# Kernel tuning notes

Hardware: AMD Instinct MI355X
Metric: run time of the kernel (lower is better)

The kernel has to match this reference:

```python
import jax, jax.numpy as jnp
import numpy as np

NUM_HEADS = 16
THETA = 10000.0


def _rope(x, cos, sin):
    # x: [B, H, S, d_k]; cos/sin: [S, d_k//2]
    x_even = x[..., 0::2]
    x_odd = x[..., 1::2]
    out_even = x_even * cos - x_odd * sin
    out_odd = x_odd * cos + x_even * sin
    # interleave back to original even/odd layout
    return jnp.stack([out_even, out_odd], axis=-1).reshape(x.shape)


def setup_inputs() -> dict:
    key = jax.random.key(0)
    ks = jax.random.split(key, 5)
    B, S, D = 2, 2048, 1024
    std = 2.0 / (D + D)
    return {
        "x": jax.random.normal(ks[0], (B, S, D), dtype=jnp.float32),
        "w_q": jax.random.normal(ks[1], (D, D), dtype=jnp.float32) * std,
        "w_k": jax.random.normal(ks[2], (D, D), dtype=jnp.float32) * std,
        "w_v": jax.random.normal(ks[3], (D, D), dtype=jnp.float32) * std,
        "w_o": jax.random.normal(ks[4], (D, D), dtype=jnp.float32) * std,
    }


def reference(x, w_q, w_k, w_v, w_o):
    B, S, D = x.shape
    H = NUM_HEADS
    d_k = D // H

    # QKV projections: x @ W.T
    q = jnp.einsum('bsd,ed->bse', x, w_q).reshape(B, S, H, d_k).transpose(0, 2, 1, 3)
    k = jnp.einsum('bsd,ed->bse', x, w_k).reshape(B, S, H, d_k).transpose(0, 2, 1, 3)
    v = jnp.einsum('bsd,ed->bse', x, w_v).reshape(B, S, H, d_k).transpose(0, 2, 1, 3)

    # RoPE (token_positions = arange(S))
    pos = jnp.arange(S, dtype=jnp.float32)
    inv_freq = 1.0 / (THETA ** (2.0 * jnp.arange(d_k // 2, dtype=jnp.float32) / d_k))
    angles = pos[:, None] * inv_freq[None, :]  # [S, d_k//2]
    cos, sin = jnp.cos(angles), jnp.sin(angles)
    q = _rope(q, cos, sin)
    k = _rope(k, cos, sin)

    # causal attention
    scores = jnp.einsum('bhqd,bhkd->bhqk', q, k) / jnp.sqrt(jnp.float32(d_k))
    causal = jnp.tril(jnp.ones((S, S), dtype=bool))
    scores = jnp.where(causal[None, None], scores, -jnp.inf)
    attn = jax.nn.softmax(scores, axis=-1)
    out = jnp.einsum('bhqk,bhkd->bhqd', attn, v)  # [B, H, S, d_k]

    out = out.transpose(0, 2, 1, 3).reshape(B, S, D)
    return jnp.einsum('bsd,ed->bse', out, w_o)
```

## Files before the change

### kernel.cpp

```cpp
#include <hip/hip_runtime.h>

typedef unsigned short u16;
typedef unsigned int u32;
typedef short bf16x8 __attribute__((ext_vector_type(8)));
typedef float f32x4 __attribute__((ext_vector_type(4)));

#define CSC 0.18033688011112042f

__device__ __forceinline__ u16 f2bf(float f) {
    union { float f; unsigned u; } x; x.f = f;
    unsigned r = x.u + 0x7fffu + ((x.u >> 16) & 1u);
    return (u16)(r >> 16);
}
__device__ __forceinline__ float bf2f(u16 v) {
    union { unsigned u; float f; } x; x.u = ((unsigned)v) << 16;
    return x.f;
}
__device__ __forceinline__ u32 cvt_pk_bf16(float lo, float hi) {
    u32 r;
    asm("v_cvt_pk_bf16_f32 %0, %1, %2" : "=v"(r) : "v"(lo), "v"(hi));
    return r;
}
__device__ __forceinline__ float exp2_fast(float x) {
#if __has_builtin(__builtin_amdgcn_exp2f)
    return __builtin_amdgcn_exp2f(x);
#else
    return exp2f(x);
#endif
}
__device__ __forceinline__ void gl_lds16(const u16* g, u16* l) {
#if __has_builtin(__builtin_amdgcn_global_load_lds)
    __builtin_amdgcn_global_load_lds(
        (const __attribute__((address_space(1))) unsigned int*)g,
        (__attribute__((address_space(3))) unsigned int*)l, 16, 0, 0);
#else
    *(bf16x8*)l = *(const bf16x8*)g;
#endif
}
__device__ __forceinline__ int ileave(int x) {
    return (x < 16) ? (x << 1) : (((x - 16) << 1) | 1);
}

__global__ void cvt_all_kernel(const float* __restrict__ x, const float* __restrict__ wq,
                               const float* __restrict__ wk, const float* __restrict__ wv,
                               const float* __restrict__ wo,
                               u16* __restrict__ xb, u16* __restrict__ qkvw,
                               u16* __restrict__ ow) {
    int i = blockIdx.x * 256 + threadIdx.x;
    const float4* src;
    ushort4* dst;
    if (i < 1048576) {
        src = (const float4*)x + i;
        dst = (ushort4*)xb + i;
    } else {
        int r = i - 1048576;
        int m = r >> 18;
        int off = r & 262143;
        const float* s4 = (m == 0) ? wq : (m == 1) ? wk : (m == 2) ? wv : wo;
        u16* d = (m < 3) ? (qkvw + (size_t)m * 1048576) : ow;
        src = (const float4*)s4 + off;
        dst = (ushort4*)d + off;
    }
    float4 v = *src;
    ushort4 o;
    o.x = f2bf(v.x); o.y = f2bf(v.y); o.z = f2bf(v.z); o.w = f2bf(v.w);
    *dst = o;
}

__global__ void rope_kernel(u16* __restrict__ qb, u16* __restrict__ kb) {
    int idx = blockIdx.x * 256 + threadIdx.x;
    u16* buf;
    float scale;
    if (blockIdx.y == 0) { buf = qb; scale = CSC; } else { buf = kb; scale = 1.0f; }
    int g   = idx & 7;
    int row = idx >> 3;
    int s   = row & 2047;
    u16* p = buf + (size_t)row * 64 + g * 8;
    bf16x8 v = *(bf16x8*)p;
    bf16x8 o;
    #pragma unroll
    for (int q = 0; q < 4; ++q) {
        int i = g * 4 + q;
        float inv = exp2_fast((float)i * -0.4152410118609203f);
        float ang = (float)s * inv;
        float sn, cs;
        sincosf(ang, &sn, &cs);
        float e  = bf2f(((u16*)&v)[2 * q]);
        float od = bf2f(((u16*)&v)[2 * q + 1]);
        ((u16*)&o)[2 * q]     = f2bf((e * cs - od * sn) * scale);
        ((u16*)&o)[2 * q + 1] = f2bf((od * cs + e * sn) * scale);
    }
    *(bf16x8*)p = o;
}

__global__ __launch_bounds__(256) void gemm_qkv(const u16* __restrict__ A,
                                                const u16* __restrict__ Bw,
                                                u16* __restrict__ C, int K) {
    __shared__ __align__(16) u16 SB[16384];
    u16* SH = SB;
    const int tid  = threadIdx.x;
    const int bm   = blockIdx.x * 128;
    const int bn   = blockIdx.y * 128;
    const int wave = tid >> 6, lane = tid & 63;
    const int wm   = (wave >> 1) * 64, wn = (wave & 1) * 64;
    const int l16  = lane & 15, quad = lane >> 4;
    const int mat  = bn >> 10;

    f32x4 acc[4][4];
    #pragma unroll
    for (int i = 0; i < 4; i++)
        #pragma unroll
        for (int j = 0; j < 4; j++)
            #pragma unroll
            for (int e = 0; e < 4; e++) acc[i][j][e] = 0.0f;

    const int srow = tid >> 2;
    const int scol = (((tid & 3) ^ ((tid >> 3) & 3))) * 8;
    const u16* gA0 = A  + (size_t)(bm + srow) * K + scol;
    const u16* gA1 = A  + (size_t)(bm + 64 + srow) * K + scol;
    const u16* gB0 = Bw + (size_t)(bn + srow) * K + scol;
    const u16* gB1 = Bw + (size_t)(bn + 64 + srow) * K + scol;
    const int csw = (quad ^ ((l16 >> 1) & 3)) * 8;

    auto stage = [&](int k0, int buf) {
        u16* As = SB + buf * 8192;
        u16* Bs = As + 4096;
        gl_lds16(gA0 + k0, As + (size_t)tid * 8);
        gl_lds16(gA1 + k0, As + (size_t)(tid + 256) * 8);
        gl_lds16(gB0 + k0, Bs + (size_t)tid * 8);
        gl_lds16(gB1 + k0, Bs + (size_t)(tid + 256) * 8);
    };

    stage(0, 0);
    int cur = 0;
    for (int k0 = 0; k0 < K; k0 += 32) {
        __syncthreads();
        if (k0 + 32 < K) stage(k0 + 32, cur ^ 1);
        const u16* As = SB + cur * 8192;
        const u16* Bs = As + 4096;
        bf16x8 af[4], bfr[4];
        #pragma unroll
        for (int i = 0; i < 4; i++) af[i]  = *(const bf16x8*)&As[(wm + i * 16 + l16) * 32 + csw];
        #pragma unroll
        for (int j = 0; j < 4; j++) bfr[j] = *(const bf16x8*)&Bs[(wn + j * 16 + l16) * 32 + csw];
        #pragma unroll
        for (int i = 0; i < 4; i++)
            #pragma unroll
            for (int j = 0; j < 4; j++)
                acc[i][j] = __builtin_amdgcn_mfma_f32_16x16x32_bf16(af[i], bfr[j], acc[i][j], 0, 0, 0);
        cur ^= 1;
    }

    const int b  = bm >> 11, sb = bm & 2047;
    if (mat < 2) {
        #pragma unroll
        for (int pass = 0; pass < 2; ++pass) {
            __syncthreads();
            if ((wn >> 6) == pass) {
                #pragma unroll
                for (int i = 0; i < 4; i++)
                    #pragma unroll
                    for (int j = 0; j < 4; j++)
                        #pragma unroll
                        for (int r = 0; r < 4; r++) {
                            int rl = wm + i * 16 + quad * 4 + r;
                            int cl = j * 16 + l16;
                            SH[rl * 66 + cl] = f2bf(acc[i][j][r]);
                        }
            }
            __syncthreads();
            int rl   = tid >> 1;
            int half = (tid & 1) * 32;
            int c    = (bn + pass * 64) & 1023;
            int h    = c >> 6;
            int s    = sb + rl;
            u16* dst = C + (size_t)mat * 4194304 +
                       (((size_t)(b * 16 + h) * 2048 + s) * 64) + half;
            const u16* srcp = &SH[rl * 66 + half];
            #pragma unroll
            for (int kk = 0; kk < 4; ++kk)
                *(bf16x8*)(dst + kk * 8) = *(const bf16x8*)(srcp + kk * 8);
        }
    } else {
        #pragma unroll
        for (int pass = 0; pass < 2; ++pass) {
            __syncthreads();
            if ((wn >> 6) == pass) {
                #pragma unroll
                for (int i = 0; i < 4; i++)
                    #pragma unroll
                    for (int j = 0; j < 4; j++)
                        #pragma unroll
                        for (int r = 0; r < 4; r++) {
                            int row = j * 16 + l16;
                            int ml  = wm + i * 16 + quad * 4 + r;
                            int sp  = (ml & ~31) | ileave(ml & 31);
                            SH[row * 130 + sp] = f2bf(acc[i][j][r]);
                        }
            }
            __syncthreads();
            int row = tid >> 2, seg = tid & 3;
            int cc  = (bn + pass * 64 + row) & 1023;
            int h = cc >> 6, dv = cc & 63;
            u16* dst = C + (size_t)8388608 +
                       (((size_t)(b * 16 + h) * 64 + dv) * 2048) + sb + seg * 32;
            const u16* srcp = &SH[row * 130 + seg * 32];
            #pragma unroll
            for (int kk = 0; kk < 4; ++kk)
                *(bf16x8*)(dst + kk * 8) = *(const bf16x8*)(srcp + kk * 8);
        }
    }
}

__global__ __launch_bounds__(256, 2) void gemm_out(const u16* __restrict__ A,
                                                   const u16* __restrict__ Bw,
                                                   float* __restrict__ C, int K) {
    __shared__ __align__(16) u16 SB[12288];
    const int tid  = threadIdx.x;
    const int bm   = blockIdx.x * 128;
    const int bn   = blockIdx.y * 64;
    const int wave = tid >> 6, lane = tid & 63;
    const int wm   = wave * 32;
    const int l16  = lane & 15, quad = lane >> 4;

    f32x4 acc[2][4];
    #pragma unroll
    for (int i = 0; i < 2; i++)
        #pragma unroll
        for (int j = 0; j < 4; j++)
            #pragma unroll
            for (int e = 0; e < 4; e++) acc[i][j][e] = 0.0f;

    const int srow = tid >> 2;
    const int scol = (((tid & 3) ^ ((tid >> 3) & 3))) * 8;
    const u16* gA0 = A  + (size_t)(bm + srow) * K + scol;
    const u16* gA1 = A  + (size_t)(bm + 64 + srow) * K + scol;
    const u16* gB0 = Bw + (size_t)(bn + srow) * K + scol;
    const int csw = (quad ^ ((l16 >> 1) & 3)) * 8;

    auto stage = [&](int k0, int buf) {
        u16* base = SB + buf * 6144;
        gl_lds16(gA0 + k0, base + (size_t)tid * 8);
        gl_lds16(gA1 + k0, base + (size_t)(tid + 256) * 8);
        gl_lds16(gB0 + k0, base + 4096 + (size_t)tid * 8);
    };

    stage(0, 0);
    int cur = 0;
    for (int k0 = 0; k0 < K; k0 += 32) {
        __syncthreads();
        if (k0 + 32 < K) stage(k0 + 32, cur ^ 1);
        const u16* As = SB + cur * 6144;
        const u16* Bs = As + 4096;
        bf16x8 af[2], bfr[4];
        #pragma unroll
        for (int i = 0; i < 2; i++) af[i]  = *(const bf16x8*)&As[(wm + i * 16 + l16) * 32 + csw];
        #pragma unroll
        for (int j = 0; j < 4; j++) bfr[j] = *(const bf16x8*)&Bs[(j * 16 + l16) * 32 + csw];
        #pragma unroll
        for (int i = 0; i < 2; i++)
            #pragma unroll
            for (int j = 0; j < 4; j++)
                acc[i][j] = __builtin_amdgcn_mfma_f32_16x16x32_bf16(af[i], bfr[j], acc[i][j], 0, 0, 0);
        cur ^= 1;
    }

    #pragma unroll
    for (int i = 0; i < 2; i++)
        #pragma unroll
        for (int j = 0; j < 4; j++)
            #pragma unroll
            for (int r = 0; r < 4; r++) {
                int mr = bm + wm + i * 16 + quad * 4 + r;
                int nc = bn + j * 16 + l16;
                C[(size_t)mr * 1024 + nc] = acc[i][j][r];
            }
}

__global__ __launch_bounds__(256, 2) void attn_kernel(const u16* __restrict__ Q,
                                                      const u16* __restrict__ Kb,
                                                      const u16* __restrict__ Vt,
                                                      u16* __restrict__ Oout) {
    __shared__ __align__(16) u16 KV[2][8192];
    __shared__ __align__(16) u16 PW[8 * 1024];
    const int tid  = threadIdx.x;
    const int wave = tid >> 6, lane = tid & 63;
    const int l16  = lane & 15, quad = lane >> 4;
    const int bid  = blockIdx.x;
    const int j    = (bid >> 3) & 15;
    const int bh   = (bid & 7) * 4 + (bid >> 7);
    const int T    = 32 - j;
    const int qA0  = j * 64 + wave * 16;
    const int qB0  = (31 - j) * 64 + wave * 16;

    const u16* Qh = Q  + (size_t)bh * 2048 * 64;
    const u16* Kh = Kb + (size_t)bh * 2048 * 64;
    const u16* Vh = Vt + (size_t)bh * 64 * 2048;

    bf16x8 qAf0 = *(const bf16x8*)&Qh[(size_t)(qA0 + l16) * 64 + quad * 8];
    bf16x8 qAf1 = *(const bf16x8*)&Qh[(size_t)(qA0 + l16) * 64 + 32 + quad * 8];
    bf16x8 qBf0 = *(const bf16x8*)&Qh[(size_t)(qB0 + l16) * 64 + quad * 8];
    bf16x8 qBf1 = *(const bf16x8*)&Qh[(size_t)(qB0 + l16) * 64 + 32 + quad * 8];

    f32x4 oA[4], oB[4];
    float lsA[4], lsB[4];
    #pragma unroll
    for (int t = 0; t < 4; t++)
        #pragma unroll
        for (int e = 0; e < 4; e++) { oA[t][e] = 0.0f; oB[t][e] = 0.0f; }
    #pragma unroll
    for (int r = 0; r < 4; r++) { lsA[r] = 0.0f; lsB[r] = 0.0f; }

    const int srow = tid >> 2;
    const int scs  = (((tid & 3) ^ ((tid >> 3) & 3))) * 8;
    const u16* gK = Kh + (size_t)srow * 64 + scs;
    const u16* gV = Vh + (size_t)srow * 2048 + scs;

    const int cswz = (quad ^ ((l16 >> 1) & 3)) * 8;
    const int psw0 = ((quad ^ (l16 & 7)) << 3);
    const int psw1 = (((quad ^ (l16 & 7)) ^ 4) << 3);

    u16* pw16B = PW + wave * 2048;
    u16* pw16A = pw16B + 1024;
    u32* pw32B = (u32*)pw16B;
    u32* pw32A = (u32*)pw16A;

    auto stage = [&](int t, int buf) {
        u16* base = KV[buf];
        gl_lds16(gK + (size_t)t * 4096,      base + (size_t)tid * 8);
        gl_lds16(gK + (size_t)t * 4096 + 32, base + 2048 + (size_t)tid * 8);
        gl_lds16(gV + (size_t)t * 64,        base + 4096 + (size_t)tid * 8);
        gl_lds16(gV + (size_t)t * 64 + 32,   base + 6144 + (size_t)tid * 8);
    };

    auto qk_pack = [&](const bf16x8& q0f, const bf16x8& q1f, bf16x8* kf0, bf16x8* kf1,
                       float* ls, u32* pw32, int q0, int kbase, bool diag) {
        f32x4 s[4];
        #pragma unroll
        for (int n = 0; n < 4; n++) {
            #pragma unroll
            for (int e = 0; e < 4; e++) s[n][e] = 0.0f;
            s[n] = __builtin_amdgcn_mfma_f32_16x16x32_bf16(q0f, kf0[n], s[n], 0, 0, 0);
            s[n] = __builtin_amdgcn_mfma_f32_16x16x32_bf16(q1f, kf1[n], s[n], 0, 0, 0);
        }
        float p[4][4];
        #pragma unroll
        for (int n = 0; n < 4; n++)
            #pragma unroll
            for (int r = 0; r < 4; r++) {
                float v = exp2_fast(s[n][r]);
                if (diag) {
                    int row = q0 + quad * 4 + r;
                    v = (kbase + n * 16 + l16 > row) ? 0.0f : v;
                }
                p[n][r] = v;
                ls[r] += v;
            }
        #pragma unroll
        for (int c = 0; c < 2; c++)
            #pragma unroll
            for (int r = 0; r < 4; r++) {
                int prow = quad * 4 + r;
                int pj   = (((c * 4 + (l16 >> 2)) ^ (prow & 7)) << 2) | (l16 & 3);
                pw32[prow * 32 + pj] = cvt_pk_bf16(p[2 * c][r], p[2 * c + 1][r]);
            }
    };

    auto pv = [&](u16* pw16, bf16x8* vf0, bf16x8* vf1, f32x4* o) {
        bf16x8 pf0 = *(const bf16x8*)&pw16[l16 * 64 + psw0];
        bf16x8 pf1 = *(const bf16x8*)&pw16[l16 * 64 + psw1];
        #pragma unroll
        for (int dn = 0; dn < 4; dn++) {
            o[dn] = __builtin_amdgcn_mfma_f32_16x16x32_bf16(pf0, vf0[dn], o[dn], 0, 0, 0);
            o[dn] = __builtin_amdgcn_mfma_f32_16x16x32_bf16(pf1, vf1[dn], o[dn], 0, 0, 0);
        }
    };

    stage(0, 0);
    for (int t = 0; t < T; ++t) {
        __syncthreads();
        if (t + 1 < T) stage(t + 1, (t + 1) & 1);
        const u16* B = KV[t & 1];
        bf16x8 kf0[4], kf1[4], vf0[4], vf1[4];
        #pragma unroll
        for (int n = 0; n < 4; n++) {
            int ri = (n * 16 + l16) * 32 + cswz;
            kf0[n] = *(const bf16x8*)&B[ri];
            kf1[n] = *(const bf16x8*)&B[2048 + ri];
            vf0[n] = *(const bf16x8*)&B[4096 + ri];
            vf1[n] = *(const bf16x8*)&B[6144 + ri];
        }
        const int kbase = t * 64;
        const bool hasA = (t <= j);

        qk_pack(qBf0, qBf1, kf0, kf1, lsB, pw32B, qB0, kbase, t == T - 1);
        if (hasA)
            qk_pack(qAf0, qAf1, kf0, kf1, lsA, pw32A, qA0, kbase, t == j);

        asm volatile("s_waitcnt lgkmcnt(0)" ::: "memory");

        pv(pw16B, vf0, vf1, oB);
        if (hasA)
            pv(pw16A, vf0, vf1, oA);
    }

    #pragma unroll
    for (int off = 1; off < 16; off <<= 1)
        #pragma unroll
        for (int r = 0; r < 4; r++) {
            lsA[r] += __shfl_xor(lsA[r], off);
            lsB[r] += __shfl_xor(lsB[r], off);
        }

    const int b = bh >> 4, h = bh & 15;
    #pragma unroll
    for (int r = 0; r < 4; r++) {
        float iA = 1.0f / lsA[r];
        float iB = 1.0f / lsB[r];
        int sA = qA0 + quad * 4 + r;
        int sB = qB0 + quad * 4 + r;
        #pragma unroll
        for (int dn = 0; dn < 4; dn++) {
            int d = h * 64 + dn * 16 + l16;
            Oout[((size_t)b * 2048 + sA) * 1024 + d] = f2bf(oA[dn][r] * iA);
            Oout[((size_t)b * 2048 + sB) * 1024 + d] = f2bf(oB[dn][r] * iB);
        }
    }
}

extern "C" void kernel_launch(void* const* d_in, const int* in_sizes, int n_in,
                              void* d_out, int out_size, void* d_ws, size_t ws_size,
                              hipStream_t stream) {
    const float* x  = (const float*)d_in[0];
    const float* wq = (const float*)d_in[1];
    const float* wk = (const float*)d_in[2];
    const float* wv = (const float*)d_in[3];
    const float* wo = (const float*)d_in[4];
    float* out = (float*)d_out;

    const int M = 4096, D = 1024;
    u16* xb    = (u16*)d_ws;
    u16* qkvw  = xb   + (size_t)M * D;
    u16* ow    = qkvw + (size_t)3 * D * D;
    u16* qkv   = ow   + (size_t)D * D;
    u16* qb    = qkv;
    u16* kb    = qkv + (size_t)M * D;
    u16* vtb   = qkv + (size_t)2 * M * D;
    u16* aob   = qkv + (size_t)3 * M * D;

    cvt_all_kernel<<<8192, 256, 0, stream>>>(x, wq, wk, wv, wo, xb, qkvw, ow);

    dim3 gq(32, 24);
    gemm_qkv<<<gq, 256, 0, stream>>>(xb, qkvw, qkv, D);

    dim3 gr(2048, 2);
    rope_kernel<<<gr, 256, 0, stream>>>(qb, kb);

    attn_kernel<<<512, 256, 0, stream>>>(qb, kb, vtb, aob);

    dim3 go(32, 16);
    gemm_out<<<go, 256, 0, stream>>>(aob, ow, out, D);
}
```

Before: 183.6 us.

## Software-pipeline PV of previous tile with QK of current tile

Double-buffers the per-wave P scratch in shared memory and defers each tile's P·V MFMAs to the next iteration, so they run alongside the current tile's QK and exp work. This removes the explicit lgkmcnt wait between writing P and reading it back. In exchange, V fragments for the previous tile are carried in extra registers and the P scratch doubles in size, which may raise register pressure and hurt occupancy at launch bounds of 2.

```diff
diff --git a/kernel.cpp b/kernel.cpp
--- a/kernel.cpp
+++ b/kernel.cpp
@@ -282,7 +282,7 @@
                                                       const u16* __restrict__ Vt,
                                                       u16* __restrict__ Oout) {
     __shared__ __align__(16) u16 KV[2][8192];
-    __shared__ __align__(16) u16 PW[8 * 1024];
+    __shared__ __align__(16) u16 PW[4 * 4096];
     const int tid  = threadIdx.x;
     const int wave = tid >> 6, lane = tid & 63;
     const int l16  = lane & 15, quad = lane >> 4;
@@ -320,10 +320,7 @@
     const int psw0 = ((quad ^ (l16 & 7)) << 3);
     const int psw1 = (((quad ^ (l16 & 7)) ^ 4) << 3);
 
-    u16* pw16B = PW + wave * 2048;
-    u16* pw16A = pw16B + 1024;
-    u32* pw32B = (u32*)pw16B;
-    u32* pw32A = (u32*)pw16A;
+    u16* pwBase = PW + wave * 4096;
 
     auto stage = [&](int t, int buf) {
         u16* base = KV[buf];
@@ -366,7 +363,7 @@
             }
     };
 
-    auto pv = [&](u16* pw16, bf16x8* vf0, bf16x8* vf1, f32x4* o) {
+    auto pv = [&](const u16* pw16, bf16x8* vf0, bf16x8* vf1, f32x4* o) {
         bf16x8 pf0 = *(const bf16x8*)&pw16[l16 * 64 + psw0];
         bf16x8 pf1 = *(const bf16x8*)&pw16[l16 * 64 + psw1];
         #pragma unroll
@@ -375,6 +372,9 @@
             o[dn] = __builtin_amdgcn_mfma_f32_16x16x32_bf16(pf1, vf1[dn], o[dn], 0, 0, 0);
         }
     };
+
+    bf16x8 vfp0[4], vfp1[4];
+    bool prevA = false;
 
     stage(0, 0);
     for (int t = 0; t < T; ++t) {
@@ -390,18 +390,30 @@
             vf0[n] = *(const bf16x8*)&B[4096 + ri];
             vf1[n] = *(const bf16x8*)&B[6144 + ri];
         }
+
+        if (t > 0) {
+            const u16* pp = pwBase + ((t - 1) & 1) * 2048;
+            pv(pp, vfp0, vfp1, oB);
+            if (prevA) pv(pp + 1024, vfp0, vfp1, oA);
+        }
+
         const int kbase = t * 64;
         const bool hasA = (t <= j);
-
-        qk_pack(qBf0, qBf1, kf0, kf1, lsB, pw32B, qB0, kbase, t == T - 1);
+        u32* pwc = (u32*)(pwBase + (t & 1) * 2048);
+
+        qk_pack(qBf0, qBf1, kf0, kf1, lsB, pwc, qB0, kbase, t == T - 1);
         if (hasA)
-            qk_pack(qAf0, qAf1, kf0, kf1, lsA, pw32A, qA0, kbase, t == j);
-
-        asm volatile("s_waitcnt lgkmcnt(0)" ::: "memory");
-
-        pv(pw16B, vf0, vf1, oB);
-        if (hasA)
-            pv(pw16A, vf0, vf1, oA);
+            qk_pack(qAf0, qAf1, kf0, kf1, lsA, pwc + 512, qA0, kbase, t == j);
+
+        #pragma unroll
+        for (int n = 0; n < 4; n++) { vfp0[n] = vf0[n]; vfp1[n] = vf1[n]; }
+        prevA = hasA;
+    }
+
+    {
+        const u16* pp = pwBase + ((T - 1) & 1) * 2048;
+        pv(pp, vfp0, vfp1, oB);
+        if (prevA) pv(pp + 1024, vfp0, vfp1, oA);
     }
 
     #pragma unroll
```

After: 186.8 us. About the same (+1.7%).

## Split attention query tiles across two wave groups in 512-thread blocks

Applied to the files above, without the earlier changes.

The attention kernel now launches 512 threads per block. Waves 0-3 handle the late query tile and waves 4-7 handle the early one, where previously each wave processed both tiles serially. K staging is done by the first 256 threads and V staging by the rest, and each wave keeps only one set of accumulators. This raises parallelism and cuts per-wave register pressure. The cost is that the early-tile waves sit idle after their causal range ends while still joining every barrier, and the larger blocks may reduce how many blocks fit per CU.

```diff
diff --git a/kernel.cpp b/kernel.cpp
--- a/kernel.cpp
+++ b/kernel.cpp
@@ -277,7 +277,7 @@
             }
 }
 
-__global__ __launch_bounds__(256, 2) void attn_kernel(const u16* __restrict__ Q,
+__global__ __launch_bounds__(512, 2) void attn_kernel(const u16* __restrict__ Q,
                                                       const u16* __restrict__ Kb,
                                                       const u16* __restrict__ Vt,
                                                       u16* __restrict__ Oout) {
@@ -285,34 +285,35 @@
     __shared__ __align__(16) u16 PW[8 * 1024];
     const int tid  = threadIdx.x;
     const int wave = tid >> 6, lane = tid & 63;
+    const int side = wave >> 2;
+    const int wl   = wave & 3;
     const int l16  = lane & 15, quad = lane >> 4;
     const int bid  = blockIdx.x;
     const int j    = (bid >> 3) & 15;
     const int bh   = (bid & 7) * 4 + (bid >> 7);
     const int T    = 32 - j;
-    const int qA0  = j * 64 + wave * 16;
-    const int qB0  = (31 - j) * 64 + wave * 16;
+    const int q0   = (side == 0 ? (31 - j) : j) * 64 + wl * 16;
+    const int dTil = (side == 0) ? (T - 1) : j;
 
     const u16* Qh = Q  + (size_t)bh * 2048 * 64;
     const u16* Kh = Kb + (size_t)bh * 2048 * 64;
     const u16* Vh = Vt + (size_t)bh * 64 * 2048;
 
-    bf16x8 qAf0 = *(const bf16x8*)&Qh[(size_t)(qA0 + l16) * 64 + quad * 8];
-    bf16x8 qAf1 = *(const bf16x8*)&Qh[(size_t)(qA0 + l16) * 64 + 32 + quad * 8];
-    bf16x8 qBf0 = *(const bf16x8*)&Qh[(size_t)(qB0 + l16) * 64 + quad * 8];
-    bf16x8 qBf1 = *(const bf16x8*)&Qh[(size_t)(qB0 + l16) * 64 + 32 + quad * 8];
-
-    f32x4 oA[4], oB[4];
-    float lsA[4], lsB[4];
+    bf16x8 qf0 = *(const bf16x8*)&Qh[(size_t)(q0 + l16) * 64 + quad * 8];
+    bf16x8 qf1 = *(const bf16x8*)&Qh[(size_t)(q0 + l16) * 64 + 32 + quad * 8];
+
+    f32x4 o[4];
+    float ls[4];
     #pragma unroll
     for (int t = 0; t < 4; t++)
         #pragma unroll
-        for (int e = 0; e < 4; e++) { oA[t][e] = 0.0f; oB[t][e] = 0.0f; }
-    #pragma unroll
-    for (int r = 0; r < 4; r++) { lsA[r] = 0.0f; lsB[r] = 0.0f; }
-
-    const int srow = tid >> 2;
-    const int scs  = (((tid & 3) ^ ((tid >> 3) & 3))) * 8;
+        for (int e = 0; e < 4; e++) o[t][e] = 0.0f;
+    #pragma unroll
+    for (int r = 0; r < 4; r++) ls[r] = 0.0f;
+
+    const int tid2 = tid & 255;
+    const int srow = tid2 >> 2;
+    const int scs  = (((tid2 & 3) ^ ((tid2 >> 3) & 3))) * 8;
     const u16* gK = Kh + (size_t)srow * 64 + scs;
     const u16* gV = Vh + (size_t)srow * 2048 + scs;
 
@@ -320,59 +321,17 @@
     const int psw0 = ((quad ^ (l16 & 7)) << 3);
     const int psw1 = (((quad ^ (l16 & 7)) ^ 4) << 3);
 
-    u16* pw16B = PW + wave * 2048;
-    u16* pw16A = pw16B + 1024;
-    u32* pw32B = (u32*)pw16B;
-    u32* pw32A = (u32*)pw16A;
+    u16* pw16 = PW + wave * 1024;
+    u32* pw32 = (u32*)pw16;
 
     auto stage = [&](int t, int buf) {
         u16* base = KV[buf];
-        gl_lds16(gK + (size_t)t * 4096,      base + (size_t)tid * 8);
-        gl_lds16(gK + (size_t)t * 4096 + 32, base + 2048 + (size_t)tid * 8);
-        gl_lds16(gV + (size_t)t * 64,        base + 4096 + (size_t)tid * 8);
-        gl_lds16(gV + (size_t)t * 64 + 32,   base + 6144 + (size_t)tid * 8);
-    };
-
-    auto qk_pack = [&](const bf16x8& q0f, const bf16x8& q1f, bf16x8* kf0, bf16x8* kf1,
-                       float* ls, u32* pw32, int q0, int kbase, bool diag) {
-        f32x4 s[4];
-        #pragma unroll
-        for (int n = 0; n < 4; n++) {
-            #pragma unroll
-            for (int e = 0; e < 4; e++) s[n][e] = 0.0f;
-            s[n] = __builtin_amdgcn_mfma_f32_16x16x32_bf16(q0f, kf0[n], s[n], 0, 0, 0);
-            s[n] = __builtin_amdgcn_mfma_f32_16x16x32_bf16(q1f, kf1[n], s[n], 0, 0, 0);
-        }
-        float p[4][4];
-        #pragma unroll
-        for (int n = 0; n < 4; n++)
-            #pragma unroll
-            for (int r = 0; r < 4; r++) {
-                float v = exp2_fast(s[n][r]);
-                if (diag) {
-                    int row = q0 + quad * 4 + r;
-                    v = (kbase + n * 16 + l16 > row) ? 0.0f : v;
-                }
-                p[n][r] = v;
-                ls[r] += v;
-            }
-        #pragma unroll
-        for (int c = 0; c < 2; c++)
-            #pragma unroll
-            for (int r = 0; r < 4; r++) {
-                int prow = quad * 4 + r;
-                int pj   = (((c * 4 + (l16 >> 2)) ^ (prow & 7)) << 2) | (l16 & 3);
-                pw32[prow * 32 + pj] = cvt_pk_bf16(p[2 * c][r], p[2 * c + 1][r]);
-            }
-    };
-
-    auto pv = [&](u16* pw16, bf16x8* vf0, bf16x8* vf1, f32x4* o) {
-        bf16x8 pf0 = *(const bf16x8*)&pw16[l16 * 64 + psw0];
-        bf16x8 pf1 = *(const bf16x8*)&pw16[l16 * 64 + psw1];
-        #pragma unroll
-        for (int dn = 0; dn < 4; dn++) {
-            o[dn] = __builtin_amdgcn_mfma_f32_16x16x32_bf16(pf0, vf0[dn], o[dn], 0, 0, 0);
-            o[dn] = __builtin_amdgcn_mfma_f32_16x16x32_bf16(pf1, vf1[dn], o[dn], 0, 0, 0);
+        if (tid < 256) {
+            gl_lds16(gK + (size_t)t * 4096,      base + (size_t)tid2 * 8);
+            gl_lds16(gK + (size_t)t * 4096 + 32, base + 2048 + (size_t)tid2 * 8);
+        } else {
+            gl_lds16(gV + (size_t)t * 64,        base + 4096 + (size_t)tid2 * 8);
+            gl_lds16(gV + (size_t)t * 64 + 32,   base + 6144 + (size_t)tid2 * 8);
         }
     };
 
@@ -380,50 +339,76 @@
     for (int t = 0; t < T; ++t) {
         __syncthreads();
         if (t + 1 < T) stage(t + 1, (t + 1) & 1);
-        const u16* B = KV[t & 1];
-        bf16x8 kf0[4], kf1[4], vf0[4], vf1[4];
-        #pragma unroll
-        for (int n = 0; n < 4; n++) {
-            int ri = (n * 16 + l16) * 32 + cswz;
-            kf0[n] = *(const bf16x8*)&B[ri];
-            kf1[n] = *(const bf16x8*)&B[2048 + ri];
-            vf0[n] = *(const bf16x8*)&B[4096 + ri];
-            vf1[n] = *(const bf16x8*)&B[6144 + ri];
+        const bool act = (side == 0) || (t <= j);
+        if (act) {
+            const u16* B = KV[t & 1];
+            bf16x8 kf0[4], kf1[4], vf0[4], vf1[4];
+            #pragma unroll
+            for (int n = 0; n < 4; n++) {
+                int ri = (n * 16 + l16) * 32 + cswz;
+                kf0[n] = *(const bf16x8*)&B[ri];
+                kf1[n] = *(const bf16x8*)&B[2048 + ri];
+                vf0[n] = *(const bf16x8*)&B[4096 + ri];
+                vf1[n] = *(const bf16x8*)&B[6144 + ri];
+            }
+            const int kbase = t * 64;
+            const bool diag = (t == dTil);
+
+            f32x4 s[4];
+            #pragma unroll
+            for (int n = 0; n < 4; n++) {
+                #pragma unroll
+                for (int e = 0; e < 4; e++) s[n][e] = 0.0f;
+                s[n] = __builtin_amdgcn_mfma_f32_16x16x32_bf16(qf0, kf0[n], s[n], 0, 0, 0);
+                s[n] = __builtin_amdgcn_mfma_f32_16x16x32_bf16(qf1, kf1[n], s[n], 0, 0, 0);
+            }
+            float p[4][4];
+            #pragma unroll
+            for (int n = 0; n < 4; n++)
+                #pragma unroll
+                for (int r = 0; r < 4; r++) {
+                    float v = exp2_fast(s[n][r]);
+                    if (diag) {
+                        int row = q0 + quad * 4 + r;
+                        v = (kbase + n * 16 + l16 > row) ? 0.0f : v;
+                    }
+                    p[n][r] = v;
+                    ls[r] += v;
+                }
+            #pragma unroll
+            for (int c = 0; c < 2; c++)
+                #pragma unroll
+                for (int r = 0; r < 4; r++) {
+                    int prow = quad * 4 + r;
+                    int pj   = (((c * 4 + (l16 >> 2)) ^ (prow & 7)) << 2) | (l16 & 3);
+                    pw32[prow * 32 + pj] = cvt_pk_bf16(p[2 * c][r], p[2 * c + 1][r]);
+                }
+            asm volatile("s_waitcnt lgkmcnt(0)" ::: "memory");
+            bf16x8 pf0 = *(const bf16x8*)&pw16[l16 * 64 + psw0];
+            bf16x8 pf1 = *(const bf16x8*)&pw16[l16 * 64 + psw1];
+            #pragma unroll
+            for (int dn = 0; dn < 4; dn++) {
+                o[dn] = __builtin_amdgcn_mfma_f32_16x16x32_bf16(pf0, vf0[dn], o[dn], 0, 0, 0);
+                o[dn] = __builtin_amdgcn_mfma_f32_16x16x32_bf16(pf1, vf1[dn], o[dn], 0, 0, 0);
+            }
         }
-        const int kbase = t * 64;
-        const bool hasA = (t <= j);
-
-        qk_pack(qBf0, qBf1, kf0, kf1, lsB, pw32B, qB0, kbase, t == T - 1);
-        if (hasA)
-            qk_pack(qAf0, qAf1, kf0, kf1, lsA, pw32A, qA0, kbase, t == j);
-
-        asm volatile("s_waitcnt lgkmcnt(0)" ::: "memory");
-
-        pv(pw16B, vf0, vf1, oB);
-        if (hasA)
-            pv(pw16A, vf0, vf1, oA);
     }
 
     #pragma unroll
     for (int off = 1; off < 16; off <<= 1)
         #pragma unroll
-        for (int r = 0; r < 4; r++) {
-            lsA[r] += __shfl_xor(lsA[r], off);
-            lsB[r] += __shfl_xor(lsB[r], off);
-        }
+        for (int r = 0; r < 4; r++)
+            ls[r] += __shfl_xor(ls[r], off);
 
     const int b = bh >> 4, h = bh & 15;
     #pragma unroll
     for (int r = 0; r < 4; r++) {
-        float iA = 1.0f / lsA[r];
-        float iB = 1.0f / lsB[r];
-        int sA = qA0 + quad * 4 + r;
-        int sB = qB0 + quad * 4 + r;
+        float inv = 1.0f / ls[r];
+        int srw = q0 + quad * 4 + r;
         #pragma unroll
         for (int dn = 0; dn < 4; dn++) {
             int d = h * 64 + dn * 16 + l16;
-            Oout[((size_t)b * 2048 + sA) * 1024 + d] = f2bf(oA[dn][r] * iA);
-            Oout[((size_t)b * 2048 + sB) * 1024 + d] = f2bf(oB[dn][r] * iB);
+            Oout[((size_t)b * 2048 + srw) * 1024 + d] = f2bf(o[dn][r] * inv);
         }
     }
 }
@@ -454,9 +439,9 @@
     gemm_qkv<<<gq, 256, 0, stream>>>(xb, qkvw, qkv, D);
 
     dim3 gr(2048, 2);
-    rope_kernel<<<gr, 256, 0, stream>>>(qb, kb);
-
-    attn_kernel<<<512, 256, 0, stream>>>(qb, kb, vtb, aob);
+    rope_kernel<<<gr, 2048 ? 256 : 256, 0, stream>>>(qb, kb);
+
+    attn_kernel<<<512, 512, 0, stream>>>(qb, kb, vtb, aob);
 
     dim3 go(32, 16);
     gemm_out<<<go, 256, 0, stream>>>(aob, ow, out, D);
```

New measurement: 179.1 us. -2.5%, faster.
